# Kernel optimization log

Measured on AMD Instinct MI355X. Metric: run time of the kernel, lower is better.

The kernel has to match this reference:

```python
import jax, jax.numpy as jnp
import numpy as np


def _jac_det(u):
    # u: [B, 3, D, H, W] displacement field in [-1, 1]-normalized coords
    B, C, D, H, W = u.shape
    scale = jnp.array([(D - 1) / 2.0, (H - 1) / 2.0, (W - 1) / 2.0], dtype=u.dtype)
    phi = u * scale[None, :, None, None, None]
    px, py, pz = phi[:, 0], phi[:, 1], phi[:, 2]  # each [B, D, H, W]
    # torch.gradient == numpy.gradient: central differences interior, one-sided edges
    gx = lambda a: jnp.gradient(a, axis=-3)
    gy = lambda a: jnp.gradient(a, axis=-2)
    gz = lambda a: jnp.gradient(a, axis=-1)
    dxx = gx(px) + 1.0
    dxy = gy(px)
    dxz = gz(px)
    dyx = gx(py)
    dyy = gy(py) + 1.0
    dyz = gz(py)
    dzx = gx(pz)
    dzy = gy(pz)
    dzz = gz(pz) + 1.0
    det = (dxx * (dyy * dzz - dyz * dzy)
           + dxy * (dyz * dzx - dyx * dzz)
           + dxz * (dyx * dzy - dyy * dzx))
    return det


def setup_inputs() -> dict:
    key = jax.random.key(0)
    displacement_field = jax.random.normal(key, (2, 3, 160, 192, 160), dtype=jnp.float32) * 0.05
    return {"displacement_field": displacement_field}


def reference(displacement_field):
    det = _jac_det(displacement_field)
    # loss = mean(relu(-det))
    return jnp.mean(jax.nn.relu(-det))
```

## Files before the change

kernel.cpp:

```cpp
#include <hip/hip_runtime.h>

#define Dd 160
#define Hh 192
#define Ww 160
#define HW (Hh * Ww)
#define DHW ((size_t)Dd * HW)
#define NVOX_D 9830400.0

#define TH 8
#define TD 10
#define QROW (Ww / 4)
#define TPB (QROW * TH)
#define NHT (Hh / TH)
#define NDS (Dd / TD)
#define GRID1 (2 * NHT * NDS)
#define NXCD 8
#define CHUNK (GRID1 / NXCD)
#define BLK2 256

__device__ __forceinline__ float4 ld4(const float* p) {
    return *reinterpret_cast<const float4*>(p);
}

__device__ __forceinline__ float4 wgrad(float4 cc, float lft, float rgt, int w0) {
    float4 g;
    g.x = (w0 == 0)      ? (cc.y - cc.x) : 0.5f * (cc.y - lft);
    g.y = 0.5f * (cc.z - cc.x);
    g.z = 0.5f * (cc.w - cc.y);
    g.w = (w0 + 4 == Ww) ? (cc.w - cc.z) : 0.5f * (rgt - cc.z);
    return g;
}

__device__ __forceinline__ float relu_negdet(
    float gd0, float gh0, float gw0,
    float gd1, float gh1, float gw1,
    float gd2, float gh2, float gw2)
{
    const float sx = 79.5f;
    const float sy = 95.5f;
    const float sz = 79.5f;
    float dxx = fmaf(sx, gd0, 1.0f);
    float dxy = sx * gh0;
    float dxz = sx * gw0;
    float dyx = sy * gd1;
    float dyy = fmaf(sy, gh1, 1.0f);
    float dyz = sy * gw1;
    float dzx = sz * gd2;
    float dzy = sz * gh2;
    float dzz = fmaf(sz, gw2, 1.0f);
    float det = dxx * (dyy * dzz - dyz * dzy)
              + dxy * (dyz * dzx - dyx * dzz)
              + dxz * (dyx * dzy - dyy * dzx);
    return fmaxf(-det, 0.0f);
}

__global__ __launch_bounds__(TPB) void jac_partial(const float* __restrict__ u,
                                                   float* __restrict__ part)
{
    const int lg  = (blockIdx.x % NXCD) * CHUNK + blockIdx.x / NXCD;
    const int ds  = lg % NDS;
    const int ht  = (lg / NDS) % NHT;
    const int b   = lg / (NDS * NHT);

    const int tid = threadIdx.x;
    const int wq  = tid % QROW;
    const int hh  = tid / QROW;
    const int h   = ht * TH + hh;
    const int w0  = wq * 4;

    const int hm = (h > 0)      ? h - 1 : 0;
    const int hp = (h < Hh - 1) ? h + 1 : Hh - 1;
    const float hinv = 1.0f / (float)(hp - hm);
    const int offm = (hm - h) * Ww;
    const int offp = (hp - h) * Ww;

    const int d0     = ds * TD;
    const int dir    = (ds & 1) ? -1 : 1;
    const int dstart = (dir > 0) ? d0 : d0 + TD - 1;

    const float* pcA = u + (size_t)(b * 3 + 0) * DHW + (size_t)h * Ww + w0;
    const float* pcB = pcA + DHW;
    const float* pcC = pcA + 2 * DHW;

    float4 a0, a1, b0, b1, c0, c1;
    {
        int db = dstart - dir;
        db = (db < 0) ? 0 : ((db > Dd - 1) ? Dd - 1 : db);
        const size_t om = (size_t)db * HW;
        const size_t oc = (size_t)dstart * HW;
        a0 = ld4(pcA + om);  a1 = ld4(pcA + oc);
        b0 = ld4(pcB + om);  b1 = ld4(pcB + oc);
        c0 = ld4(pcC + om);  c1 = ld4(pcC + oc);
    }

    float acc = 0.0f;

    #pragma unroll 2
    for (int i = 0; i < TD; ++i) {
        const int d  = dstart + dir * i;
        int dn = d + dir;
        dn = (dn < 0) ? 0 : ((dn > Dd - 1) ? Dd - 1 : dn);
        const float dinvs = (float)dir * ((d > 0 && d < Dd - 1) ? 0.5f : 1.0f);
        const size_t od  = (size_t)d  * HW;
        const size_t odn = (size_t)dn * HW;

        float4 a2 = ld4(pcA + odn);
        float4 b2 = ld4(pcB + odn);
        float4 c2 = ld4(pcC + odn);

        const float* pdA = pcA + od;
        const float* pdB = pcB + od;
        const float* pdC = pcC + od;

        float4 rAm = ld4(pdA + offm), rAp = ld4(pdA + offp);
        float4 rBm = ld4(pdB + offm), rBp = ld4(pdB + offp);
        float4 rCm = ld4(pdC + offm), rCp = ld4(pdC + offp);

        float lA = (w0 > 0) ? pdA[-1] : 0.0f;
        float lB = (w0 > 0) ? pdB[-1] : 0.0f;
        float lC = (w0 > 0) ? pdC[-1] : 0.0f;
        float rA = (w0 + 4 < Ww) ? pdA[4] : 0.0f;
        float rB = (w0 + 4 < Ww) ? pdB[4] : 0.0f;
        float rC = (w0 + 4 < Ww) ? pdC[4] : 0.0f;

        float4 gwA = wgrad(a1, lA, rA, w0);
        float4 gwB = wgrad(b1, lB, rB, w0);
        float4 gwC = wgrad(c1, lC, rC, w0);

        float4 ghA = make_float4((rAp.x - rAm.x) * hinv, (rAp.y - rAm.y) * hinv,
                                 (rAp.z - rAm.z) * hinv, (rAp.w - rAm.w) * hinv);
        float4 ghB = make_float4((rBp.x - rBm.x) * hinv, (rBp.y - rBm.y) * hinv,
                                 (rBp.z - rBm.z) * hinv, (rBp.w - rBm.w) * hinv);
        float4 ghC = make_float4((rCp.x - rCm.x) * hinv, (rCp.y - rCm.y) * hinv,
                                 (rCp.z - rCm.z) * hinv, (rCp.w - rCm.w) * hinv);

        float4 gdA = make_float4((a2.x - a0.x) * dinvs, (a2.y - a0.y) * dinvs,
                                 (a2.z - a0.z) * dinvs, (a2.w - a0.w) * dinvs);
        float4 gdB = make_float4((b2.x - b0.x) * dinvs, (b2.y - b0.y) * dinvs,
                                 (b2.z - b0.z) * dinvs, (b2.w - b0.w) * dinvs);
        float4 gdC = make_float4((c2.x - c0.x) * dinvs, (c2.y - c0.y) * dinvs,
                                 (c2.z - c0.z) * dinvs, (c2.w - c0.w) * dinvs);

        acc += relu_negdet(gdA.x, ghA.x, gwA.x, gdB.x, ghB.x, gwB.x, gdC.x, ghC.x, gwC.x)
             + relu_negdet(gdA.y, ghA.y, gwA.y, gdB.y, ghB.y, gwB.y, gdC.y, ghC.y, gwC.y)
             + relu_negdet(gdA.z, ghA.z, gwA.z, gdB.z, ghB.z, gwB.z, gdC.z, ghC.z, gwC.z)
             + relu_negdet(gdA.w, ghA.w, gwA.w, gdB.w, ghB.w, gwB.w, gdC.w, ghC.w, gwC.w);

        a0 = a1; a1 = a2;
        b0 = b1; b1 = b2;
        c0 = c1; c1 = c2;
    }

    #pragma unroll
    for (int off = 32; off > 0; off >>= 1)
        acc += __shfl_down(acc, off, 64);
    __shared__ float sred[TPB / 64];
    const int lane = tid & 63;
    const int wid  = tid >> 6;
    if (lane == 0) sred[wid] = acc;
    __syncthreads();
    if (tid == 0)
        part[lg] = ((sred[0] + sred[1]) + (sred[2] + sred[3])) + sred[4];
}

__global__ __launch_bounds__(BLK2) void jac_final(const float* __restrict__ part,
                                                  float* __restrict__ out)
{
    const int t = threadIdx.x;
    double a = (double)part[t] + (double)part[t + 256] + (double)part[t + 512];
    __shared__ double s[BLK2];
    s[t] = a;
    __syncthreads();
    #pragma unroll
    for (int off = BLK2 / 2; off > 0; off >>= 1) {
        if (t < off) s[t] += s[t + off];
        __syncthreads();
    }
    if (t == 0)
        out[0] = (float)(s[0] / NVOX_D);
}

extern "C" void kernel_launch(void* const* d_in, const int* in_sizes, int n_in,
                              void* d_out, int out_size, void* d_ws, size_t ws_size,
                              hipStream_t stream)
{
    const float* u = (const float*)d_in[0];
    float* part = (float*)d_ws;

    jac_partial<<<GRID1, TPB, 0, stream>>>(u, part);
    jac_final<<<1, BLK2, 0, stream>>>(part, (float*)d_out);
}
```

Measured before the change: 38.02 us.

## Stage depth slices in double-buffered LDS to share H and W neighbor reads

Each depth slice for all three components, plus one halo row above and below the tile, is now written into a double-buffered shared-memory tile. H-neighbor rows and W-edge scalars are read from LDS instead of issuing extra global loads per thread. This removes redundant global/L2 traffic for the stencil (six float4 and six scalar loads per iteration). The cost is a block-wide barrier per depth step and some LDS bank traffic, which may reduce latency hiding in what was a cache-friendly memory-bound kernel.

New measurement: 42.52 us. +11.8%, slower.

```diff
diff --git a/kernel.cpp b/kernel.cpp
--- a/kernel.cpp
+++ b/kernel.cpp
@@ -16,6 +16,8 @@
 #define GRID1 (2 * NHT * NDS)
 #define NXCD 8
 #define CHUNK (GRID1 / NXCD)
+#define NWAVE (TPB / 64)
+#define NHALO (2 * QROW * 3)
 #define BLK2 256
 
 __device__ __forceinline__ float4 ld4(const float* p) {
@@ -45,9 +47,9 @@
     float dyx = sy * gd1;
     float dyy = fmaf(sy, gh1, 1.0f);
     float dyz = sy * gw1;
+    float dzz = fmaf(sz, gw2, 1.0f);
     float dzx = sz * gd2;
     float dzy = sz * gh2;
-    float dzz = fmaf(sz, gw2, 1.0f);
     float det = dxx * (dyy * dzz - dyz * dzy)
               + dxy * (dyz * dzx - dyx * dzz)
               + dxz * (dyx * dzy - dyy * dzx);
@@ -57,6 +59,9 @@
 __global__ __launch_bounds__(TPB) void jac_partial(const float* __restrict__ u,
                                                    float* __restrict__ part)
 {
+    __shared__ float4 buf[2][3][TH + 2][QROW];
+    __shared__ float sred[NWAVE];
+
     const int lg  = (blockIdx.x % NXCD) * CHUNK + blockIdx.x / NXCD;
     const int ds  = lg % NDS;
     const int ht  = (lg / NDS) % NHT;
@@ -71,8 +76,6 @@
     const int hm = (h > 0)      ? h - 1 : 0;
     const int hp = (h < Hh - 1) ? h + 1 : Hh - 1;
     const float hinv = 1.0f / (float)(hp - hm);
-    const int offm = (hm - h) * Ww;
-    const int offp = (hp - h) * Ww;
 
     const int d0     = ds * TD;
     const int dir    = (ds & 1) ? -1 : 1;
@@ -81,6 +84,15 @@
     const float* pcA = u + (size_t)(b * 3 + 0) * DHW + (size_t)h * Ww + w0;
     const float* pcB = pcA + DHW;
     const float* pcC = pcA + 2 * DHW;
+
+    const bool is_halo = (tid < NHALO);
+    const int hc   = tid / (2 * QROW);
+    const int hsel = (tid / QROW) % 2;
+    const int hwq  = tid % QROW;
+    int hrow = ht * TH + (hsel ? TH : -1);
+    hrow = (hrow < 0) ? 0 : ((hrow > Hh - 1) ? Hh - 1 : hrow);
+    const int hlrow = hsel ? TH + 1 : 0;
+    const float* phal = u + (size_t)(b * 3 + hc) * DHW + (size_t)hrow * Ww + hwq * 4;
 
     float4 a0, a1, b0, b1, c0, c1;
     {
@@ -91,37 +103,41 @@
         a0 = ld4(pcA + om);  a1 = ld4(pcA + oc);
         b0 = ld4(pcB + om);  b1 = ld4(pcB + oc);
         c0 = ld4(pcC + om);  c1 = ld4(pcC + oc);
+        buf[0][0][hh + 1][wq] = a1;
+        buf[0][1][hh + 1][wq] = b1;
+        buf[0][2][hh + 1][wq] = c1;
+        if (is_halo) buf[0][hc][hlrow][hwq] = ld4(phal + oc);
     }
+    __syncthreads();
 
     float acc = 0.0f;
 
     #pragma unroll 2
     for (int i = 0; i < TD; ++i) {
-        const int d  = dstart + dir * i;
+        const int cur = i & 1;
+        const int nxt = cur ^ 1;
+        const int d = dstart + dir * i;
         int dn = d + dir;
         dn = (dn < 0) ? 0 : ((dn > Dd - 1) ? Dd - 1 : dn);
         const float dinvs = (float)dir * ((d > 0 && d < Dd - 1) ? 0.5f : 1.0f);
-        const size_t od  = (size_t)d  * HW;
         const size_t odn = (size_t)dn * HW;
+        const bool do_stage = (i < TD - 1);
 
         float4 a2 = ld4(pcA + odn);
         float4 b2 = ld4(pcB + odn);
         float4 c2 = ld4(pcC + odn);
-
-        const float* pdA = pcA + od;
-        const float* pdB = pcB + od;
-        const float* pdC = pcC + od;
-
-        float4 rAm = ld4(pdA + offm), rAp = ld4(pdA + offp);
-        float4 rBm = ld4(pdB + offm), rBp = ld4(pdB + offp);
-        float4 rCm = ld4(pdC + offm), rCp = ld4(pdC + offp);
-
-        float lA = (w0 > 0) ? pdA[-1] : 0.0f;
-        float lB = (w0 > 0) ? pdB[-1] : 0.0f;
-        float lC = (w0 > 0) ? pdC[-1] : 0.0f;
-        float rA = (w0 + 4 < Ww) ? pdA[4] : 0.0f;
-        float rB = (w0 + 4 < Ww) ? pdB[4] : 0.0f;
-        float rC = (w0 + 4 < Ww) ? pdC[4] : 0.0f;
+        float4 hal = make_float4(0.f, 0.f, 0.f, 0.f);
+        if (do_stage && is_halo) hal = ld4(phal + odn);
+
+        float4 rAm = buf[cur][0][hh][wq],     rAp = buf[cur][0][hh + 2][wq];
+        float4 rBm = buf[cur][1][hh][wq],     rBp = buf[cur][1][hh + 2][wq];
+        float4 rCm = buf[cur][2][hh][wq],     rCp = buf[cur][2][hh + 2][wq];
+
+        const int wqm = (wq > 0) ? wq - 1 : 0;
+        const int wqp = (wq < QROW - 1) ? wq + 1 : QROW - 1;
+        float lA = buf[cur][0][hh + 1][wqm].w, rA = buf[cur][0][hh + 1][wqp].x;
+        float lB = buf[cur][1][hh + 1][wqm].w, rB = buf[cur][1][hh + 1][wqp].x;
+        float lC = buf[cur][2][hh + 1][wqm].w, rC = buf[cur][2][hh + 1][wqp].x;
 
         float4 gwA = wgrad(a1, lA, rA, w0);
         float4 gwB = wgrad(b1, lB, rB, w0);
@@ -146,6 +162,14 @@
              + relu_negdet(gdA.z, ghA.z, gwA.z, gdB.z, ghB.z, gwB.z, gdC.z, ghC.z, gwC.z)
              + relu_negdet(gdA.w, ghA.w, gwA.w, gdB.w, ghB.w, gwB.w, gdC.w, ghC.w, gwC.w);
 
+        if (do_stage) {
+            buf[nxt][0][hh + 1][wq] = a2;
+            buf[nxt][1][hh + 1][wq] = b2;
+            buf[nxt][2][hh + 1][wq] = c2;
+            if (is_halo) buf[nxt][hc][hlrow][hwq] = hal;
+            __syncthreads();
+        }
+
         a0 = a1; a1 = a2;
         b0 = b1; b1 = b2;
         c0 = c1; c1 = c2;
@@ -154,7 +178,6 @@
     #pragma unroll
     for (int off = 32; off > 0; off >>= 1)
         acc += __shfl_down(acc, off, 64);
-    __shared__ float sred[TPB / 64];
     const int lane = tid & 63;
     const int wid  = tid >> 6;
     if (lane == 0) sred[wid] = acc;
```
